# Performance work log

Hardware: AMD Instinct MI355X
Metric: run time of the kernel (lower is better)

## Reference

```python
import jax, jax.numpy as jnp
import numpy as np

ALPHA = 0.2  # module hardcodes a = 0.2


def _triplet_total(outputs, labels):
    # Faithful vectorization of the nested-loop mining:
    #  - sort samples by label (stable, like python sorted with key=label)
    #  - anchor p1 = first element of each contiguous label group
    #  - positives p2 = remaining members of the group; ap = ||p1-p2||^2
    #  - negatives = every sample with a different label
    #  - per (p2, neg): add (ap - an + alpha) for an in {||p1-n||^2, ||p2-n||^2}
    #    iff ap < an and ap - an + alpha > 0  (i.e. 0 < an - ap < alpha)
    order = jnp.argsort(labels)          # stable sort, matches python sorted
    x = outputs[order]                   # [n, d]
    lab = labels[order]                  # [n]
    n = x.shape[0]
    idx = jnp.arange(n)
    is_start = jnp.concatenate([jnp.ones((1,), bool), lab[1:] != lab[:-1]])
    # index of the group-start (anchor) for every position
    anchor_of = jax.lax.cummax(jnp.where(is_start, idx, 0))

    # pairwise squared distances Dm[i,j] = ||x_i - x_j||^2
    sq = jnp.sum(x * x, axis=-1)                       # [n]
    Dm = sq[:, None] + sq[None, :] - 2.0 * (x @ x.T)   # [n, n]

    ap = Dm[anchor_of, idx]   # [n]   ||p1 - p2||^2 for each potential positive
    an1 = Dm[anchor_of, :]    # [n,n] ||p1 - neg||^2
    an2 = Dm                  # [n,n] ||p2 - neg||^2

    pos_mask = ~is_start                         # p2 ranges over non-anchor rows
    neg_mask = lab[:, None] != lab[None, :]      # negatives: different label
    valid = pos_mask[:, None] & neg_mask         # [n, n]

    def hinge(an):
        d = ap[:, None] - an
        return jnp.where((d < 0) & (d + ALPHA > 0), d + ALPHA, 0.0)

    contrib = jnp.where(valid, hinge(an1) + hinge(an2), 0.0)
    return jnp.sum(contrib)


def setup_inputs() -> dict:
    key = jax.random.key(0)
    k1, k2 = jax.random.split(key)
    N, D, C = 8192, 128, 512
    outputs = jax.random.normal(k1, (N, D), dtype=jnp.float32)
    labels = jax.random.randint(k2, (N,), 0, C, dtype=jnp.int32)
    return {"outputs": outputs, "labels": labels}


def reference(outputs, labels):
    return _triplet_total(outputs, labels)
```

## Files before the change

kernel.cpp:

```cpp
#include <hip/hip_runtime.h>
#include <limits.h>
#include <stdint.h>

#define ALPHA 0.2f
#define HALFA 0.1f
static constexpr int N = 8192;
static constexpr int D = 128;
static constexpr int C = 512;
static constexpr int BT = 128;
static constexpr int FT = 64;
static constexpr int KC = 32;
static constexpr int SL = 40;
static constexpr int NB = N / BT;
static constexpr int NTRI = NB * (NB + 1) / 2;
static constexpr int MAXG = 64;
static constexpr int ABIAS = 0x40000000;

using half8   = __attribute__((ext_vector_type(8))) _Float16;
using floatx16 = __attribute__((ext_vector_type(16))) float;

__device__ __forceinline__ floatx16 zerov() { floatx16 v = {0.f}; return v; }

__device__ __forceinline__ half8 cvt8(float4 v0, float4 v1) {
    half8 h;
    h[0] = (_Float16)v0.x; h[1] = (_Float16)v0.y; h[2] = (_Float16)v0.z; h[3] = (_Float16)v0.w;
    h[4] = (_Float16)v1.x; h[5] = (_Float16)v1.y; h[6] = (_Float16)v1.z; h[7] = (_Float16)v1.w;
    return h;
}

__device__ __forceinline__ float ss8(float4 v0, float4 v1) {
    return v0.x*v0.x + v0.y*v0.y + v0.z*v0.z + v0.w*v0.w
         + v1.x*v1.x + v1.y*v1.y + v1.z*v1.z + v1.w*v1.w;
}


__launch_bounds__(256)
__global__ void k_front(const float* __restrict__ x, const int* __restrict__ labels,
                        _Float16* __restrict__ xh, float* __restrict__ sqg,
                        int* __restrict__ anchorg, float* __restrict__ T,
                        float* __restrict__ ap, float* __restrict__ out) {
    __shared__ __align__(16) _Float16 As[FT * SL];
    __shared__ __align__(16) _Float16 Bs[FT * SL];
    __shared__ float sPartA[FT * 4];
    __shared__ float sPartB[FT * 4];
    __shared__ float sSqA[FT];
    __shared__ float sSqJ[FT];
    __shared__ int sLabJ[FT];
    __shared__ int sA[FT];

    const int cb = blockIdx.x, jb = blockIdx.y;
    const int c0 = cb * FT;
    const int j0 = jb * FT;
    const int tid = threadIdx.x;
    const int lane = tid & 63, w = tid >> 6;
    const int m = lane & 31, q = lane >> 5;
    const int wrow = (w >> 1) * 32;
    const int wcol = (w & 1) * 32;

    if (tid < FT) sA[tid] = INT_MAX;
    else if (tid < 2 * FT) sLabJ[tid - FT] = labels[j0 + tid - FT];
    __syncthreads();

    const int4* lab4 = (const int4*)labels;
    for (int t = tid; t < N / 4; t += 256) {
        int4 lv = lab4[t];
        int base = t * 4;
#pragma unroll
        for (int k = 0; k < 4; ++k) {
            int l = (k == 0) ? lv.x : (k == 1) ? lv.y : (k == 2) ? lv.z : lv.w;
            int li = l - c0;
            if ((unsigned)li < (unsigned)FT) atomicMin(&sA[li], base + k);
        }
    }
    if (cb == 0 && jb == 0 && tid == 0) out[0] = 0.f;
    __syncthreads();

    if (jb == 0 && tid < FT)
        anchorg[c0 + tid] = (sA[tid] == INT_MAX) ? -1 : (ABIAS - sA[tid]);

    floatx16 acc = zerov();
    const _Float16* Abase = &As[(wrow + m) * SL + q * 8];
    const _Float16* Bbase = &Bs[(wcol + m) * SL + q * 8];

    float ssA = 0.f, ssB = 0.f;
    const int srow = tid >> 2, sg = tid & 3;

    for (int kc = 0; kc < D; kc += KC) {
        __syncthreads();
        {
            size_t go = (size_t)kc + sg * 8;
            int ar = sA[srow]; if (ar == INT_MAX) ar = 0;
            float4 a0 = *(const float4*)(x + (size_t)ar * D + go);
            float4 a1 = *(const float4*)(x + (size_t)ar * D + go + 4);
            *(half8*)(&As[srow * SL + sg * 8]) = cvt8(a0, a1);
            ssA += ss8(a0, a1);
            float4 b0 = *(const float4*)(x + (size_t)(j0 + srow) * D + go);
            float4 b1 = *(const float4*)(x + (size_t)(j0 + srow) * D + go + 4);
            half8 hb = cvt8(b0, b1);
            *(half8*)(&Bs[srow * SL + sg * 8]) = hb;
            ssB += ss8(b0, b1);
            if (cb == 0) *(half8*)(xh + (size_t)(j0 + srow) * D + go) = hb;
        }
        __syncthreads();
#pragma unroll
        for (int ks = 0; ks < KC; ks += 16) {
            half8 a0 = *(const half8*)(Abase + ks);
            half8 b0 = *(const half8*)(Bbase + ks);
            acc = __builtin_amdgcn_mfma_f32_32x32x16_f16(a0, b0, acc, 0, 0, 0);
        }
    }

    sPartA[srow * 4 + sg] = ssA;
    sPartB[srow * 4 + sg] = ssB;
    __syncthreads();
    if (tid < FT) {
        sSqA[tid] = sPartA[tid * 4] + sPartA[tid * 4 + 1]
                  + sPartA[tid * 4 + 2] + sPartA[tid * 4 + 3];
    } else if (tid < 2 * FT) {
        int r = tid - FT;
        float s = sPartB[r * 4] + sPartB[r * 4 + 1] + sPartB[r * 4 + 2] + sPartB[r * 4 + 3];
        sSqJ[r] = s;
        if (cb == 0) sqg[j0 + r] = s;
    }
    __syncthreads();

    const int col = wcol + m;
    const float sqj = sSqJ[col];
    const int labj = sLabJ[col];

#pragma unroll
    for (int rr = 0; rr < 16; ++rr) {
        int row = wrow + (rr & 3) + 8 * (rr >> 2) + 4 * q;
        int c = c0 + row;
        float Dv = fmaf(-2.f, acc[rr], sSqA[row] + sqj);
        T[(size_t)c * N + j0 + col] = Dv;
        if (labj == c) ap[j0 + col] = Dv;
    }
}


__launch_bounds__(256)
__global__ void k_mega(const _Float16* __restrict__ xh, const int* __restrict__ labels,
                       const int* __restrict__ anchor, const float* __restrict__ sq,
                       const float* __restrict__ ap, const float* __restrict__ T,
                       float* __restrict__ out) {
    __shared__ __align__(16) _Float16 As[BT * SL];
    __shared__ __align__(16) _Float16 Bs[BT * SL];
    __shared__ float4 rowE[BT];
    __shared__ float4 colE[BT];
    __shared__ float wsum[4];

    const int tid = threadIdx.x;
    const int lane = tid & 63, w = tid >> 6;
    float local = 0.f;

    if ((int)blockIdx.x < C) {
        const int c = blockIdx.x;
        __shared__ float sge[MAXG];
        __shared__ int sglen;
        int raw = anchor[c];
        if (raw > 0) {
            int a = ABIAS - raw;
            if (tid == 0) sglen = 0;
            __syncthreads();
            for (int t = tid; t < N; t += 256) {
                if (labels[t] == c && t != a) {
                    int slot = atomicAdd(&sglen, 1);
                    if (slot < MAXG) sge[slot] = ap[t] + HALFA;
                }
            }
            __syncthreads();
            int glen = sglen; if (glen > MAXG) glen = MAXG;
            if (glen > 0) {
                const float4* trow = (const float4*)(T + (size_t)c * N);
                const int4* lrow = (const int4*)labels;
#pragma unroll 2
                for (int ch = 0; ch < 8; ++ch) {
                    float4 tv = trow[ch * 256 + tid];
                    int4 lv = lrow[ch * 256 + tid];
                    for (int g = 0; g < glen; ++g) {
                        float e = sge[g];
                        float u;
                        u = e - tv.x; if (lv.x != c && __builtin_fabsf(u) < HALFA) local += u + HALFA;
                        u = e - tv.y; if (lv.y != c && __builtin_fabsf(u) < HALFA) local += u + HALFA;
                        u = e - tv.z; if (lv.z != c && __builtin_fabsf(u) < HALFA) local += u + HALFA;
                        u = e - tv.w; if (lv.w != c && __builtin_fabsf(u) < HALFA) local += u + HALFA;
                    }
                }
            }
        }
    } else {
        int rem = blockIdx.x - C, br = 0;
        while (rem >= NB - br) { rem -= NB - br; ++br; }
        const int bc = br + rem;
        const int i0 = br * BT;
        const int j0 = bc * BT;
        const bool diag = (br == bc);
        const int wr = w >> 1, wc = w & 1;
        const int m = lane & 31, q = lane >> 5;

        if (tid < BT) {
            int i = i0 + tid;
            int li = labels[i];
            int a = ABIAS - anchor[li];
            float sqi = sq[i];
            float e2 = (i == a) ? -1e30f : ap[i] + HALFA - sqi;
            rowE[tid] = make_float4(e2, __int_as_float(li), sqi, 0.f);
        } else {
            int t = tid - BT;
            int j = j0 + t;
            int lj = labels[j];
            int a = ABIAS - anchor[lj];
            float sqj = sq[j];
            float e2 = (j == a) ? -1e30f : ap[j] + HALFA - sqj;
            colE[t] = make_float4(e2, __int_as_float(lj), sqj, 0.f);
        }

        floatx16 acc[2][2];
        acc[0][0] = zerov(); acc[0][1] = zerov(); acc[1][0] = zerov(); acc[1][1] = zerov();

        const _Float16* Abase = &As[(wr * 64 + m) * SL + q * 8];
        const _Float16* Bbase = &Bs[(wc * 64 + m) * SL + q * 8];

        for (int kc = 0; kc < D; kc += KC) {
            __syncthreads();
#pragma unroll
            for (int it = 0; it < 2; ++it) {
                int f = tid + it * 256;
                int row = f >> 2, g = f & 3;
                size_t go = (size_t)kc + g * 8;
                half8 v = *(const half8*)(xh + (size_t)(i0 + row) * D + go);
                *(half8*)(&As[row * SL + g * 8]) = v;
                half8 u = *(const half8*)(xh + (size_t)(j0 + row) * D + go);
                *(half8*)(&Bs[row * SL + g * 8]) = u;
            }
            __syncthreads();
#pragma unroll
            for (int ks = 0; ks < KC; ks += 16) {
                half8 a0 = *(const half8*)(Abase + ks);
                half8 a1 = *(const half8*)(Abase + 32 * SL + ks);
                half8 b0 = *(const half8*)(Bbase + ks);
                half8 b1 = *(const half8*)(Bbase + 32 * SL + ks);
                acc[0][0] = __builtin_amdgcn_mfma_f32_32x32x16_f16(a0, b0, acc[0][0], 0, 0, 0);
                acc[0][1] = __builtin_amdgcn_mfma_f32_32x32x16_f16(a0, b1, acc[0][1], 0, 0, 0);
                acc[1][0] = __builtin_amdgcn_mfma_f32_32x32x16_f16(a1, b0, acc[1][0], 0, 0, 0);
                acc[1][1] = __builtin_amdgcn_mfma_f32_32x32x16_f16(a1, b1, acc[1][1], 0, 0, 0);
            }
        }

        float sqj[2], e2j[2]; int labj[2];
#pragma unroll
        for (int tn = 0; tn < 2; ++tn) {
            float4 cj = colE[wc * 64 + tn * 32 + m];
            e2j[tn] = cj.x; labj[tn] = __float_as_int(cj.y); sqj[tn] = cj.z;
        }

#pragma unroll
        for (int tm = 0; tm < 2; ++tm) {
            int rbase = wr * 64 + tm * 32 + 4 * q;
#pragma unroll
            for (int rr = 0; rr < 16; ++rr) {
                int row = rbase + (rr & 3) + 8 * (rr >> 2);
                float4 re = rowE[row];
                float e2i = re.x, sqi = re.z;
                int labi = __float_as_int(re.y);
#pragma unroll
                for (int tn = 0; tn < 2; ++tn) {
                    if (labi != labj[tn]) {
                        float dot = acc[tm][tn][rr];
                        float u2 = fmaf(2.f, dot, e2i - sqj[tn]);
                        if (__builtin_fabsf(u2) < HALFA) local += u2 + HALFA;
                        if (!diag) {
                            float u2b = fmaf(2.f, dot, e2j[tn] - sqi);
                            if (__builtin_fabsf(u2b) < HALFA) local += u2b + HALFA;
                        }
                    }
                }
            }
        }
    }

#pragma unroll
    for (int off = 32; off; off >>= 1) local += __shfl_down(local, off);
    if (lane == 0) wsum[w] = local;
    __syncthreads();
    if (tid == 0) atomicAdd(out, wsum[0] + wsum[1] + wsum[2] + wsum[3]);
}


extern "C" void kernel_launch(void* const* d_in, const int* in_sizes, int n_in,
                              void* d_out, int out_size, void* d_ws, size_t ws_size,
                              hipStream_t stream) {
    const float* x = (const float*)d_in[0];
    const int* labels = (const int*)d_in[1];
    float* out = (float*)d_out;

    char* p = (char*)d_ws;
    int* anchor = (int*)p;            p += C * 4;
    float* sq = (float*)p;            p += N * 4;
    float* ap = (float*)p;            p += N * 4;
    p = (char*)(((uintptr_t)p + 255) & ~(uintptr_t)255);
    float* T = (float*)p;             p += (size_t)C * N * 4;
    _Float16* xh = (_Float16*)p;

    dim3 gf(C / FT, N / FT);
    k_front<<<gf, 256, 0, stream>>>(x, labels, xh, sq, anchor, T, ap, out);
    k_mega<<<C + NTRI, 256, 0, stream>>>(xh, labels, anchor, sq, ap, T, out);
}
```

Before: 115.9 us.

## Drop anchor-distance matrix T; fuse anchor-negative hinge into GEMM tiles

The 16 MB fp32 anchor-by-sample distance matrix T is no longer written and re-read. The anchor-negative hinge terms are now evaluated directly from MFMA accumulators in fused tiles, and each tile gathers its per-class positive lists into shared memory. Conversion to fp16, squared norms and anchor-positive distances move into two small prep kernels. Both GEMM paths now read fragments straight from global memory instead of staging through LDS. This trades a large memory round trip for an extra kernel launch and duplicated per-tile label scans with LDS atomics.

Result: slower. 142.3 us (+22.9%).

```diff
diff --git a/kernel.cpp b/kernel.cpp
--- a/kernel.cpp
+++ b/kernel.cpp
@@ -7,16 +7,14 @@
 static constexpr int N = 8192;
 static constexpr int D = 128;
 static constexpr int C = 512;
+static constexpr int MAXG = 64;
+static constexpr int FT = 64;
+static constexpr int NT1 = (C / FT) * (N / FT);
 static constexpr int BT = 128;
-static constexpr int FT = 64;
-static constexpr int KC = 32;
-static constexpr int SL = 40;
 static constexpr int NB = N / BT;
 static constexpr int NTRI = NB * (NB + 1) / 2;
-static constexpr int MAXG = 64;
-static constexpr int ABIAS = 0x40000000;
-
-using half8   = __attribute__((ext_vector_type(8))) _Float16;
+
+using half8    = __attribute__((ext_vector_type(8))) _Float16;
 using floatx16 = __attribute__((ext_vector_type(16))) float;
 
 __device__ __forceinline__ floatx16 zerov() { floatx16 v = {0.f}; return v; }
@@ -35,174 +33,162 @@
 
 
 __launch_bounds__(256)
-__global__ void k_front(const float* __restrict__ x, const int* __restrict__ labels,
-                        _Float16* __restrict__ xh, float* __restrict__ sqg,
-                        int* __restrict__ anchorg, float* __restrict__ T,
-                        float* __restrict__ ap, float* __restrict__ out) {
-    __shared__ __align__(16) _Float16 As[FT * SL];
-    __shared__ __align__(16) _Float16 Bs[FT * SL];
-    __shared__ float sPartA[FT * 4];
-    __shared__ float sPartB[FT * 4];
+__global__ void k_prep(const float* __restrict__ x, _Float16* __restrict__ xh,
+                       float* __restrict__ sq, float* __restrict__ out) {
+    const int tid = threadIdx.x;
+    if (blockIdx.x == 0 && tid == 0) out[0] = 0.f;
+    const int r = blockIdx.x * 128 + (tid >> 1);
+    const int h = tid & 1;
+    const float4* src = (const float4*)(x + (size_t)r * D + h * 64);
+    half8* dst = (half8*)(xh + (size_t)r * D + h * 64);
+    float ss = 0.f;
+#pragma unroll
+    for (int i = 0; i < 8; ++i) {
+        float4 v0 = src[2 * i], v1 = src[2 * i + 1];
+        dst[i] = cvt8(v0, v1);
+        ss += ss8(v0, v1);
+    }
+    ss += __shfl_xor(ss, 1);
+    if (h == 0) sq[r] = ss;
+}
+
+
+__launch_bounds__(256)
+__global__ void k_ap(const _Float16* __restrict__ xh, const int* __restrict__ labels,
+                     const float* __restrict__ sq, int* __restrict__ anchorg,
+                     float* __restrict__ ap) {
+    __shared__ int sAnc[C];
+    const int tid = threadIdx.x;
+    for (int i = tid; i < C; i += 256) sAnc[i] = INT_MAX;
+    __syncthreads();
+    const int4* lab4 = (const int4*)labels;
+    for (int t = tid; t < N / 4; t += 256) {
+        int4 lv = lab4[t];
+        int base = 4 * t;
+        atomicMin(&sAnc[lv.x], base);
+        atomicMin(&sAnc[lv.y], base + 1);
+        atomicMin(&sAnc[lv.z], base + 2);
+        atomicMin(&sAnc[lv.w], base + 3);
+    }
+    __syncthreads();
+    if (tid < 8) {
+        int c = blockIdx.x * 8 + tid;
+        int a = sAnc[c];
+        anchorg[c] = (a == INT_MAX) ? -1 : a;
+    }
+    const int jj = blockIdx.x * 128 + (tid >> 1);
+    const int hk = tid & 1;
+    const int lj = labels[jj];
+    const int a = sAnc[lj];
+    const half8* xa = (const half8*)(xh + (size_t)a * D + hk * 64);
+    const half8* xj = (const half8*)(xh + (size_t)jj * D + hk * 64);
+    float dot = 0.f;
+#pragma unroll
+    for (int i = 0; i < 8; ++i) {
+        half8 va = xa[i], vj = xj[i];
+#pragma unroll
+        for (int e = 0; e < 8; ++e) dot = fmaf((float)va[e], (float)vj[e], dot);
+    }
+    dot += __shfl_xor(dot, 1);
+    if (hk == 0) ap[jj] = sq[a] + sq[jj] - 2.f * dot;
+}
+
+
+__launch_bounds__(256, 2)
+__global__ void k_main(const _Float16* __restrict__ xh, const int* __restrict__ labels,
+                       const int* __restrict__ anchor, const float* __restrict__ sq,
+                       const float* __restrict__ ap, float* __restrict__ out) {
+    __shared__ float4 rowE[BT];
+    __shared__ float4 colE[BT];
+    __shared__ float sge[FT * MAXG];
+    __shared__ int   sCnt[FT];
+    __shared__ int   sArow[FT];
     __shared__ float sSqA[FT];
     __shared__ float sSqJ[FT];
-    __shared__ int sLabJ[FT];
-    __shared__ int sA[FT];
-
-    const int cb = blockIdx.x, jb = blockIdx.y;
-    const int c0 = cb * FT;
-    const int j0 = jb * FT;
+    __shared__ int   sLabJ[FT];
+    __shared__ float wsum[4];
+
     const int tid = threadIdx.x;
     const int lane = tid & 63, w = tid >> 6;
     const int m = lane & 31, q = lane >> 5;
-    const int wrow = (w >> 1) * 32;
-    const int wcol = (w & 1) * 32;
-
-    if (tid < FT) sA[tid] = INT_MAX;
-    else if (tid < 2 * FT) sLabJ[tid - FT] = labels[j0 + tid - FT];
-    __syncthreads();
-
-    const int4* lab4 = (const int4*)labels;
-    for (int t = tid; t < N / 4; t += 256) {
-        int4 lv = lab4[t];
-        int base = t * 4;
-#pragma unroll
-        for (int k = 0; k < 4; ++k) {
-            int l = (k == 0) ? lv.x : (k == 1) ? lv.y : (k == 2) ? lv.z : lv.w;
-            int li = l - c0;
-            if ((unsigned)li < (unsigned)FT) atomicMin(&sA[li], base + k);
-        }
-    }
-    if (cb == 0 && jb == 0 && tid == 0) out[0] = 0.f;
-    __syncthreads();
-
-    if (jb == 0 && tid < FT)
-        anchorg[c0 + tid] = (sA[tid] == INT_MAX) ? -1 : (ABIAS - sA[tid]);
-
-    floatx16 acc = zerov();
-    const _Float16* Abase = &As[(wrow + m) * SL + q * 8];
-    const _Float16* Bbase = &Bs[(wcol + m) * SL + q * 8];
-
-    float ssA = 0.f, ssB = 0.f;
-    const int srow = tid >> 2, sg = tid & 3;
-
-    for (int kc = 0; kc < D; kc += KC) {
+    float local = 0.f;
+
+    if ((int)blockIdx.x < NT1) {
+        const int cb = blockIdx.x >> 7;
+        const int jb = blockIdx.x & 127;
+        const int c0 = cb * FT, j0 = jb * FT;
+        const int wrow = (w >> 1) * 32, wcol = (w & 1) * 32;
+
+        if (tid < FT) {
+            int a = anchor[c0 + tid];
+            int ar = (a < 0) ? 0 : a;
+            sArow[tid] = ar;
+            sSqA[tid] = sq[ar];
+            sCnt[tid] = 0;
+        } else if (tid < 2 * FT) {
+            int j = j0 + tid - FT;
+            sLabJ[tid - FT] = labels[j];
+            sSqJ[tid - FT] = sq[j];
+        }
         __syncthreads();
-        {
-            size_t go = (size_t)kc + sg * 8;
-            int ar = sA[srow]; if (ar == INT_MAX) ar = 0;
-            float4 a0 = *(const float4*)(x + (size_t)ar * D + go);
-            float4 a1 = *(const float4*)(x + (size_t)ar * D + go + 4);
-            *(half8*)(&As[srow * SL + sg * 8]) = cvt8(a0, a1);
-            ssA += ss8(a0, a1);
-            float4 b0 = *(const float4*)(x + (size_t)(j0 + srow) * D + go);
-            float4 b1 = *(const float4*)(x + (size_t)(j0 + srow) * D + go + 4);
-            half8 hb = cvt8(b0, b1);
-            *(half8*)(&Bs[srow * SL + sg * 8]) = hb;
-            ssB += ss8(b0, b1);
-            if (cb == 0) *(half8*)(xh + (size_t)(j0 + srow) * D + go) = hb;
-        }
-        __syncthreads();
-#pragma unroll
-        for (int ks = 0; ks < KC; ks += 16) {
-            half8 a0 = *(const half8*)(Abase + ks);
-            half8 b0 = *(const half8*)(Bbase + ks);
-            acc = __builtin_amdgcn_mfma_f32_32x32x16_f16(a0, b0, acc, 0, 0, 0);
-        }
-    }
-
-    sPartA[srow * 4 + sg] = ssA;
-    sPartB[srow * 4 + sg] = ssB;
-    __syncthreads();
-    if (tid < FT) {
-        sSqA[tid] = sPartA[tid * 4] + sPartA[tid * 4 + 1]
-                  + sPartA[tid * 4 + 2] + sPartA[tid * 4 + 3];
-    } else if (tid < 2 * FT) {
-        int r = tid - FT;
-        float s = sPartB[r * 4] + sPartB[r * 4 + 1] + sPartB[r * 4 + 2] + sPartB[r * 4 + 3];
-        sSqJ[r] = s;
-        if (cb == 0) sqg[j0 + r] = s;
-    }
-    __syncthreads();
-
-    const int col = wcol + m;
-    const float sqj = sSqJ[col];
-    const int labj = sLabJ[col];
-
-#pragma unroll
-    for (int rr = 0; rr < 16; ++rr) {
-        int row = wrow + (rr & 3) + 8 * (rr >> 2) + 4 * q;
-        int c = c0 + row;
-        float Dv = fmaf(-2.f, acc[rr], sSqA[row] + sqj);
-        T[(size_t)c * N + j0 + col] = Dv;
-        if (labj == c) ap[j0 + col] = Dv;
-    }
-}
-
-
-__launch_bounds__(256)
-__global__ void k_mega(const _Float16* __restrict__ xh, const int* __restrict__ labels,
-                       const int* __restrict__ anchor, const float* __restrict__ sq,
-                       const float* __restrict__ ap, const float* __restrict__ T,
-                       float* __restrict__ out) {
-    __shared__ __align__(16) _Float16 As[BT * SL];
-    __shared__ __align__(16) _Float16 Bs[BT * SL];
-    __shared__ float4 rowE[BT];
-    __shared__ float4 colE[BT];
-    __shared__ float wsum[4];
-
-    const int tid = threadIdx.x;
-    const int lane = tid & 63, w = tid >> 6;
-    float local = 0.f;
-
-    if ((int)blockIdx.x < C) {
-        const int c = blockIdx.x;
-        __shared__ float sge[MAXG];
-        __shared__ int sglen;
-        int raw = anchor[c];
-        if (raw > 0) {
-            int a = ABIAS - raw;
-            if (tid == 0) sglen = 0;
-            __syncthreads();
-            for (int t = tid; t < N; t += 256) {
-                if (labels[t] == c && t != a) {
-                    int slot = atomicAdd(&sglen, 1);
-                    if (slot < MAXG) sge[slot] = ap[t] + HALFA;
-                }
-            }
-            __syncthreads();
-            int glen = sglen; if (glen > MAXG) glen = MAXG;
-            if (glen > 0) {
-                const float4* trow = (const float4*)(T + (size_t)c * N);
-                const int4* lrow = (const int4*)labels;
-#pragma unroll 2
-                for (int ch = 0; ch < 8; ++ch) {
-                    float4 tv = trow[ch * 256 + tid];
-                    int4 lv = lrow[ch * 256 + tid];
-                    for (int g = 0; g < glen; ++g) {
-                        float e = sge[g];
-                        float u;
-                        u = e - tv.x; if (lv.x != c && __builtin_fabsf(u) < HALFA) local += u + HALFA;
-                        u = e - tv.y; if (lv.y != c && __builtin_fabsf(u) < HALFA) local += u + HALFA;
-                        u = e - tv.z; if (lv.z != c && __builtin_fabsf(u) < HALFA) local += u + HALFA;
-                        u = e - tv.w; if (lv.w != c && __builtin_fabsf(u) < HALFA) local += u + HALFA;
+
+        const int4* lab4 = (const int4*)labels;
+        for (int t = tid; t < N / 4; t += 256) {
+            int4 lv = lab4[t];
+            int base = 4 * t;
+#pragma unroll
+            for (int kk = 0; kk < 4; ++kk) {
+                int l = (kk == 0) ? lv.x : (kk == 1) ? lv.y : (kk == 2) ? lv.z : lv.w;
+                int li = l - c0;
+                if ((unsigned)li < (unsigned)FT) {
+                    int idx = base + kk;
+                    if (idx != sArow[li]) {
+                        int slot = atomicAdd(&sCnt[li], 1);
+                        if (slot < MAXG) sge[li * MAXG + slot] = ap[idx] + HALFA;
                     }
                 }
             }
         }
+        __syncthreads();
+
+        const int arow = sArow[wrow + m];
+        const half8* Apt = (const half8*)(xh + (size_t)arow * D) + q;
+        const half8* Bpt = (const half8*)(xh + (size_t)(j0 + wcol + m) * D) + q;
+        floatx16 acc = zerov();
+#pragma unroll
+        for (int k = 0; k < D / 16; ++k) {
+            half8 av = Apt[2 * k];
+            half8 bv = Bpt[2 * k];
+            acc = __builtin_amdgcn_mfma_f32_32x32x16_f16(av, bv, acc, 0, 0, 0);
+        }
+
+        const int col = wcol + m;
+        const float sqj = sSqJ[col];
+        const int labj = sLabJ[col];
+#pragma unroll
+        for (int rr = 0; rr < 16; ++rr) {
+            int row = wrow + (rr & 3) + 8 * (rr >> 2) + 4 * q;
+            if (labj != c0 + row) {
+                float Dv = fmaf(-2.f, acc[rr], sSqA[row] + sqj);
+                int n = sCnt[row]; n = (n > MAXG) ? MAXG : n;
+                for (int g = 0; g < n; ++g) {
+                    float u = sge[row * MAXG + g] - Dv;
+                    if (__builtin_fabsf(u) < HALFA) local += u + HALFA;
+                }
+            }
+        }
     } else {
-        int rem = blockIdx.x - C, br = 0;
+        int rem = blockIdx.x - NT1, br = 0;
         while (rem >= NB - br) { rem -= NB - br; ++br; }
         const int bc = br + rem;
-        const int i0 = br * BT;
-        const int j0 = bc * BT;
+        const int i0 = br * BT, j0 = bc * BT;
         const bool diag = (br == bc);
         const int wr = w >> 1, wc = w & 1;
-        const int m = lane & 31, q = lane >> 5;
 
         if (tid < BT) {
             int i = i0 + tid;
             int li = labels[i];
-            int a = ABIAS - anchor[li];
+            int a = anchor[li];
             float sqi = sq[i];
             float e2 = (i == a) ? -1e30f : ap[i] + HALFA - sqi;
             rowE[tid] = make_float4(e2, __int_as_float(li), sqi, 0.f);
@@ -210,49 +196,37 @@
             int t = tid - BT;
             int j = j0 + t;
             int lj = labels[j];
-            int a = ABIAS - anchor[lj];
+            int a = anchor[lj];
             float sqj = sq[j];
             float e2 = (j == a) ? -1e30f : ap[j] + HALFA - sqj;
             colE[t] = make_float4(e2, __int_as_float(lj), sqj, 0.f);
         }
+        __syncthreads();
 
         floatx16 acc[2][2];
         acc[0][0] = zerov(); acc[0][1] = zerov(); acc[1][0] = zerov(); acc[1][1] = zerov();
 
-        const _Float16* Abase = &As[(wr * 64 + m) * SL + q * 8];
-        const _Float16* Bbase = &Bs[(wc * 64 + m) * SL + q * 8];
-
-        for (int kc = 0; kc < D; kc += KC) {
-            __syncthreads();
-#pragma unroll
-            for (int it = 0; it < 2; ++it) {
-                int f = tid + it * 256;
-                int row = f >> 2, g = f & 3;
-                size_t go = (size_t)kc + g * 8;
-                half8 v = *(const half8*)(xh + (size_t)(i0 + row) * D + go);
-                *(half8*)(&As[row * SL + g * 8]) = v;
-                half8 u = *(const half8*)(xh + (size_t)(j0 + row) * D + go);
-                *(half8*)(&Bs[row * SL + g * 8]) = u;
-            }
-            __syncthreads();
-#pragma unroll
-            for (int ks = 0; ks < KC; ks += 16) {
-                half8 a0 = *(const half8*)(Abase + ks);
-                half8 a1 = *(const half8*)(Abase + 32 * SL + ks);
-                half8 b0 = *(const half8*)(Bbase + ks);
-                half8 b1 = *(const half8*)(Bbase + 32 * SL + ks);
-                acc[0][0] = __builtin_amdgcn_mfma_f32_32x32x16_f16(a0, b0, acc[0][0], 0, 0, 0);
-                acc[0][1] = __builtin_amdgcn_mfma_f32_32x32x16_f16(a0, b1, acc[0][1], 0, 0, 0);
-                acc[1][0] = __builtin_amdgcn_mfma_f32_32x32x16_f16(a1, b0, acc[1][0], 0, 0, 0);
-                acc[1][1] = __builtin_amdgcn_mfma_f32_32x32x16_f16(a1, b1, acc[1][1], 0, 0, 0);
-            }
-        }
-
-        float sqj[2], e2j[2]; int labj[2];
+        const half8* A0 = (const half8*)(xh + (size_t)(i0 + wr * 64 + m) * D) + q;
+        const half8* A1 = A0 + 32 * (D / 8);
+        const half8* B0 = (const half8*)(xh + (size_t)(j0 + wc * 64 + m) * D) + q;
+        const half8* B1 = B0 + 32 * (D / 8);
+#pragma unroll
+        for (int k = 0; k < D / 16; ++k) {
+            half8 a0 = A0[2 * k];
+            half8 a1 = A1[2 * k];
+            half8 b0 = B0[2 * k];
+            half8 b1 = B1[2 * k];
+            acc[0][0] = __builtin_amdgcn_mfma_f32_32x32x16_f16(a0, b0, acc[0][0], 0, 0, 0);
+            acc[0][1] = __builtin_amdgcn_mfma_f32_32x32x16_f16(a0, b1, acc[0][1], 0, 0, 0);
+            acc[1][0] = __builtin_amdgcn_mfma_f32_32x32x16_f16(a1, b0, acc[1][0], 0, 0, 0);
+            acc[1][1] = __builtin_amdgcn_mfma_f32_32x32x16_f16(a1, b1, acc[1][1], 0, 0, 0);
+        }
+
+        float sqjv[2], e2j[2]; int labj[2];
 #pragma unroll
         for (int tn = 0; tn < 2; ++tn) {
             float4 cj = colE[wc * 64 + tn * 32 + m];
-            e2j[tn] = cj.x; labj[tn] = __float_as_int(cj.y); sqj[tn] = cj.z;
+            e2j[tn] = cj.x; labj[tn] = __float_as_int(cj.y); sqjv[tn] = cj.z;
         }
 
 #pragma unroll
@@ -268,7 +242,7 @@
                 for (int tn = 0; tn < 2; ++tn) {
                     if (labi != labj[tn]) {
                         float dot = acc[tm][tn][rr];
-                        float u2 = fmaf(2.f, dot, e2i - sqj[tn]);
+                        float u2 = fmaf(2.f, dot, e2i - sqjv[tn]);
                         if (__builtin_fabsf(u2) < HALFA) local += u2 + HALFA;
                         if (!diag) {
                             float u2b = fmaf(2.f, dot, e2j[tn] - sqi);
@@ -296,14 +270,13 @@
     float* out = (float*)d_out;
 
     char* p = (char*)d_ws;
-    int* anchor = (int*)p;            p += C * 4;
-    float* sq = (float*)p;            p += N * 4;
-    float* ap = (float*)p;            p += N * 4;
+    int* anchor = (int*)p;        p += C * 4;
+    float* sq = (float*)p;        p += N * 4;
+    float* ap = (float*)p;        p += N * 4;
     p = (char*)(((uintptr_t)p + 255) & ~(uintptr_t)255);
-    float* T = (float*)p;             p += (size_t)C * N * 4;
     _Float16* xh = (_Float16*)p;
 
-    dim3 gf(C / FT, N / FT);
-    k_front<<<gf, 256, 0, stream>>>(x, labels, xh, sq, anchor, T, ap, out);
-    k_mega<<<C + NTRI, 256, 0, stream>>>(xh, labels, anchor, sq, ap, T, out);
-}
+    k_prep<<<N / 128, 256, 0, stream>>>(x, xh, sq, out);
+    k_ap<<<N / 128, 256, 0, stream>>>(xh, labels, sq, anchor, ap);
+    k_main<<<NT1 + NTRI, 256, 0, stream>>>(xh, labels, anchor, sq, ap, out);
+}
```
